# Kernel optimization log

Measured on AMD Instinct MI355X. Metric: run time of the kernel, lower is better.

Reference implementation:

```python
import jax, jax.numpy as jnp
import numpy as np

GRAPH_SIZE = 1024
D_MODEL = 256
BATCH = 32
INITIAL_ALPHA = 1.0


def setup_inputs() -> dict:
    key = jax.random.key(0)
    ks = jax.random.split(key, 10)
    s = 1.0 / np.sqrt(D_MODEL)  # torch Linear default init scale
    inp = {
        "query": jax.random.normal(ks[0], (BATCH, GRAPH_SIZE, D_MODEL), jnp.float32),
        "key_": jax.random.normal(ks[1], (BATCH, GRAPH_SIZE, D_MODEL), jnp.float32),
        "value": jax.random.normal(ks[2], (BATCH, GRAPH_SIZE, D_MODEL), jnp.float32),
        "dist": jax.random.uniform(ks[3], (BATCH, GRAPH_SIZE, GRAPH_SIZE), jnp.float32),
        "Wq": jax.random.uniform(ks[4], (D_MODEL, D_MODEL), jnp.float32, -s, s),
        "bq": jax.random.uniform(ks[5], (D_MODEL,), jnp.float32, -s, s),
        "Wk": jax.random.uniform(ks[6], (D_MODEL, D_MODEL), jnp.float32, -s, s),
        "bk": jax.random.uniform(ks[7], (D_MODEL,), jnp.float32, -s, s),
        "Wv": jax.random.uniform(ks[8], (D_MODEL, D_MODEL), jnp.float32, -s, s),
        "bv": jax.random.uniform(ks[9], (D_MODEL,), jnp.float32, -s, s),
        # alpha_raw = exp(initial_alpha - 1)
        "alpha_raw": jnp.asarray(np.exp(INITIAL_ALPHA - 1.0), jnp.float32),
    }
    return inp


def reference(query, key_, value, dist, Wq, bq, Wk, bk, Wv, bv, alpha_raw):
    # self-attention path: mask=None, cross=False, query_size == graph_size
    log2_N = jnp.log2(jnp.asarray(GRAPH_SIZE, jnp.float32))
    alpha = jax.nn.softplus(alpha_raw) + 1e-6

    q = jnp.einsum('bnd,ed->bne', query, Wq) + bq   # fc_q
    k = jnp.einsum('bnd,ed->bne', key_, Wk) + bk    # fc_k
    v = jnp.einsum('bnd,ed->bne', value, Wv) + bv   # fc_v

    exp_A = jnp.exp(-alpha * log2_N * dist)         # [b, n, n]
    exp_K = jnp.exp(k)                              # [b, n, d]

    numerator = jnp.einsum('bqk,bkd->bqd', exp_A, exp_K * v)
    denominator = jnp.einsum('bqk,bkd->bqd', exp_A, exp_K) + 1e-8
    return jax.nn.sigmoid(q) * (numerator / denominator)
```

## Files before the change

kernel.cpp:

```cpp
#include <hip/hip_runtime.h>
#include <hip/hip_bf16.h>

#define NBATCH 32
#define NG 1024
#define DM 256
#define HB 16

typedef short bf16x8 __attribute__((ext_vector_type(8)));
typedef float f32x4 __attribute__((ext_vector_type(4)));
typedef unsigned short u16x4 __attribute__((ext_vector_type(4)));
typedef unsigned short u16x8 __attribute__((ext_vector_type(8)));

static __device__ __forceinline__ unsigned short f2bf(float f) {
    __hip_bfloat16 h = __float2bfloat16(f);
    return *reinterpret_cast<unsigned short*>(&h);
}

static __device__ __forceinline__ void gload16(const void* g, void* l) {
    __builtin_amdgcn_global_load_lds(
        (const __attribute__((address_space(1))) unsigned int*)g,
        (__attribute__((address_space(3))) unsigned int*)l, 16, 0, 0);
}

__global__ __launch_bounds__(256) void wpack_kernel(
    const float* __restrict__ Wq, const float* __restrict__ Wk,
    const float* __restrict__ Wv, unsigned short* __restrict__ Wb)
{
    const int i4 = (blockIdx.x * 256 + threadIdx.x) * 4;
    const int t = i4 >> 16;
    const int off = i4 & 65535;
    const float* src = (t == 0) ? Wq : (t == 1) ? Wk : Wv;
    float4 v = *(const float4*)(src + off);
    *(u16x4*)(Wb + i4) = (u16x4){ f2bf(v.x), f2bf(v.y), f2bf(v.z), f2bf(v.w) };
}

__global__ __launch_bounds__(256) void conv_kernel(
    const float* __restrict__ src, unsigned short* __restrict__ dst)
{
    const size_t i8 = ((size_t)blockIdx.x * 256 + threadIdx.x) * 8;
    float4 a = *(const float4*)(src + i8);
    float4 b = *(const float4*)(src + i8 + 4);
    *(u16x8*)(dst + i8) = (u16x8){ f2bf(a.x), f2bf(a.y), f2bf(a.z), f2bf(a.w),
                                   f2bf(b.x), f2bf(b.y), f2bf(b.z), f2bf(b.w) };
}

__global__ __launch_bounds__(256) void projq_kernel(
    const unsigned short* __restrict__ Xq,
    const unsigned short* __restrict__ Wb,
    const float* __restrict__ bq,
    float* __restrict__ sigq)
{
    __shared__ __align__(128) unsigned short lds[2][2][128 * 64];

    const int bid = blockIdx.x;
    const int mt = bid >> 1, nt = bid & 1;
    const int tid = threadIdx.x;
    const int w = tid >> 6, lane = tid & 63;
    const int wm = w >> 1, wn = w & 1;
    const int l15 = lane & 15, lhi = lane >> 4;
    const int lr = lane >> 3, sl = lane & 7;
    const int sp = sl ^ lr;

    const char* Abase = (const char*)(Xq + (size_t)mt * 128 * 256);
    const char* Wbase = (const char*)(Wb + (size_t)nt * 128 * 256);

    f32x4 acc[4][4];
    #pragma unroll
    for (int mi = 0; mi < 4; ++mi)
        #pragma unroll
        for (int ni = 0; ni < 4; ++ni)
            acc[mi][ni] = (f32x4){0.f, 0.f, 0.f, 0.f};

    auto STAGE = [&](int buf, int t) {
        #pragma unroll
        for (int i = 0; i < 4; ++i) {
            const int r = w * 32 + i * 8 + lr;
            gload16(Abase + (size_t)r * 512 + t * 128 + sp * 16,
                    (char*)&lds[buf][0][0] + w * 4096 + i * 1024);
            gload16(Wbase + (size_t)r * 512 + t * 128 + sp * 16,
                    (char*)&lds[buf][1][0] + w * 4096 + i * 1024);
        }
    };

    STAGE(0, 0);
    __syncthreads();

    int cur = 0;
    for (int t = 0; t < 4; ++t) {
        if (t < 3) STAGE(cur ^ 1, t + 1);
        const char* Ab = (const char*)&lds[cur][0][0];
        const char* Bb = (const char*)&lds[cur][1][0];
        #pragma unroll
        for (int kk = 0; kk < 2; ++kk) {
            bf16x8 af[4], bfr[4];
            #pragma unroll
            for (int mi = 0; mi < 4; ++mi) {
                const int tr = wm * 64 + mi * 16 + l15;
                af[mi] = *(const bf16x8*)(Ab + ((tr * 128 + kk * 64 + lhi * 16) ^ ((tr & 7) << 4)));
            }
            #pragma unroll
            for (int ni = 0; ni < 4; ++ni) {
                const int tr = wn * 64 + ni * 16 + l15;
                bfr[ni] = *(const bf16x8*)(Bb + ((tr * 128 + kk * 64 + lhi * 16) ^ ((tr & 7) << 4)));
            }
            #pragma unroll
            for (int mi = 0; mi < 4; ++mi)
                #pragma unroll
                for (int ni = 0; ni < 4; ++ni)
                    acc[mi][ni] = __builtin_amdgcn_mfma_f32_16x16x32_bf16(
                        af[mi], bfr[ni], acc[mi][ni], 0, 0, 0);
        }
        __syncthreads();
        cur ^= 1;
    }

    #pragma unroll
    for (int ni = 0; ni < 4; ++ni) {
        const int c = nt * 128 + wn * 64 + ni * 16 + l15;
        const float bqs = bq[c];
        #pragma unroll
        for (int mi = 0; mi < 4; ++mi)
            #pragma unroll
            for (int r = 0; r < 4; ++r) {
                const size_t R = (size_t)mt * 128 + wm * 64 + mi * 16 + lhi * 4 + r;
                const float qv = acc[mi][ni][r] + bqs;
                sigq[R * DM + c] = 1.0f / (1.0f + __expf(-qv));
            }
    }
}

__global__ __launch_bounds__(256) void projkv_kernel(
    const unsigned short* __restrict__ Xk,
    const unsigned short* __restrict__ Xv,
    const unsigned short* __restrict__ Wkb,
    const unsigned short* __restrict__ Wvb,
    const float* __restrict__ bk, const float* __restrict__ bv,
    unsigned short* __restrict__ Pt)
{
    __shared__ __align__(128) unsigned short lds[2][2][128 * 64];

    const int bid = blockIdx.x;
    const int mt = bid >> 1, nt = bid & 1;
    const int tid = threadIdx.x;
    const int w = tid >> 6, lane = tid & 63;
    const int wm = w >> 1, wn = w & 1;
    const int l15 = lane & 15, lhi = lane >> 4;
    const int lr = lane >> 3, sl = lane & 7;
    const int sp = sl ^ lr;
    const int g16 = (sp & 3) * 16;

    f32x4 kacc[4][4], vacc[4][4];
    #pragma unroll
    for (int mi = 0; mi < 4; ++mi)
        #pragma unroll
        for (int ni = 0; ni < 4; ++ni) {
            kacc[mi][ni] = (f32x4){0.f, 0.f, 0.f, 0.f};
            vacc[mi][ni] = (f32x4){0.f, 0.f, 0.f, 0.f};
        }

    auto STAGE = [&](int buf, int t) {
        #pragma unroll
        for (int i = 0; i < 4; ++i) {
            const int r = w * 32 + i * 8 + lr;
            const char* asrc = (sp < 4 ? (const char*)Xk : (const char*)Xv)
                               + (size_t)(mt * 128 + r) * 512 + t * 64 + g16;
            gload16(asrc, (char*)&lds[buf][0][0] + w * 4096 + i * 1024);
            const char* wsrc = (sp < 4 ? (const char*)Wkb : (const char*)Wvb)
                               + (size_t)(nt * 128 + r) * 512 + t * 64 + g16;
            gload16(wsrc, (char*)&lds[buf][1][0] + w * 4096 + i * 1024);
        }
    };

    STAGE(0, 0);
    __syncthreads();

    int cur = 0;
    for (int t = 0; t < 8; ++t) {
        if (t < 7) STAGE(cur ^ 1, t + 1);
        const char* Ab = (const char*)&lds[cur][0][0];
        const char* Bb = (const char*)&lds[cur][1][0];
        bf16x8 kaf[4], vaf[4], kbf[4], vbf[4];
        #pragma unroll
        for (int mi = 0; mi < 4; ++mi) {
            const int tr = wm * 64 + mi * 16 + l15;
            const int sw = (tr & 7) << 4;
            kaf[mi] = *(const bf16x8*)(Ab + ((tr * 128 + lhi * 16) ^ sw));
            vaf[mi] = *(const bf16x8*)(Ab + ((tr * 128 + 64 + lhi * 16) ^ sw));
        }
        #pragma unroll
        for (int ni = 0; ni < 4; ++ni) {
            const int tr = wn * 64 + ni * 16 + l15;
            const int sw = (tr & 7) << 4;
            kbf[ni] = *(const bf16x8*)(Bb + ((tr * 128 + lhi * 16) ^ sw));
            vbf[ni] = *(const bf16x8*)(Bb + ((tr * 128 + 64 + lhi * 16) ^ sw));
        }
        #pragma unroll
        for (int mi = 0; mi < 4; ++mi)
            #pragma unroll
            for (int ni = 0; ni < 4; ++ni) {
                kacc[mi][ni] = __builtin_amdgcn_mfma_f32_16x16x32_bf16(
                    kaf[mi], kbf[ni], kacc[mi][ni], 0, 0, 0);
                vacc[mi][ni] = __builtin_amdgcn_mfma_f32_16x16x32_bf16(
                    vaf[mi], vbf[ni], vacc[mi][ni], 0, 0, 0);
            }
        __syncthreads();
        cur ^= 1;
    }

    const int b = (mt * 128) >> 10;
    const int kb0 = (mt * 128) & 1023;
    #pragma unroll
    for (int ni = 0; ni < 4; ++ni) {
        const int c = nt * 128 + wn * 64 + ni * 16 + l15;
        const float bks = bk[c], bvs = bv[c];
        #pragma unroll
        for (int mi = 0; mi < 4; ++mi) {
            unsigned short p1[4], p2[4];
            #pragma unroll
            for (int r = 0; r < 4; ++r) {
                const float ek = __expf(kacc[mi][ni][r] + bks);
                const float vv = vacc[mi][ni][r] + bvs;
                p1[r] = f2bf(ek * vv);
                p2[r] = f2bf(ek);
            }
            const int kidx = kb0 + wm * 64 + mi * 16 + lhi * 4;
            *(u16x4*)&Pt[((size_t)b * 512 + 2 * c    ) * NG + kidx] =
                (u16x4){p1[0], p1[1], p1[2], p1[3]};
            *(u16x4*)&Pt[((size_t)b * 512 + 2 * c + 1) * NG + kidx] =
                (u16x4){p2[0], p2[1], p2[2], p2[3]};
        }
    }
}

__global__ __launch_bounds__(256) void exp_kernel(
    const float* __restrict__ dist, unsigned short* __restrict__ ea,
    const float* __restrict__ alpha_raw)
{
    const float alpha = log1pf(__expf(alpha_raw[0])) + 1e-6f;
    const float sc = -alpha * 10.0f * 1.44269504088896f;
    const size_t i8 = ((size_t)blockIdx.x * 256 + threadIdx.x) * 8;
    float4 v0 = *(const float4*)(dist + i8);
    float4 v1 = *(const float4*)(dist + i8 + 4);
    u16x8 o = { f2bf(exp2f(sc * v0.x)), f2bf(exp2f(sc * v0.y)),
                f2bf(exp2f(sc * v0.z)), f2bf(exp2f(sc * v0.w)),
                f2bf(exp2f(sc * v1.x)), f2bf(exp2f(sc * v1.y)),
                f2bf(exp2f(sc * v1.z)), f2bf(exp2f(sc * v1.w)) };
    *(u16x8*)(ea + i8) = o;
}

__global__ __launch_bounds__(256) void attn_kernel(
    const unsigned short* __restrict__ ea,
    const unsigned short* __restrict__ Pt,
    float* __restrict__ out)
{
    __shared__ __align__(128) unsigned short lds[2][2][128 * 64];

    const int bid = blockIdx.x;
    const int l = (bid & 7) * 64 + (bid >> 3);
    const int b = l >> 5;
    const int m = (l >> 2) & 7;
    const int n = l & 3;

    const int tid = threadIdx.x;
    const int w = tid >> 6, lane = tid & 63;
    const int wm = w >> 1, wn = w & 1;
    const int l15 = lane & 15, lhi = lane >> 4;
    const int lr = lane >> 3, cb = lane & 7;
    const int cbs = cb ^ lr;

    const char* Abase = (const char*)(ea + ((size_t)b * NG + m * 128) * NG);
    const char* Bbase = (const char*)(Pt + ((size_t)b * 512 + n * 128) * NG);

    f32x4 acc[4][4];
    #pragma unroll
    for (int mi = 0; mi < 4; ++mi)
        #pragma unroll
        for (int ni = 0; ni < 4; ++ni)
            acc[mi][ni] = (f32x4){0.f, 0.f, 0.f, 0.f};

    auto STAGE = [&](int buf, int t) {
        #pragma unroll
        for (int i = 0; i < 4; ++i) {
            const int r = w * 32 + i * 8 + lr;
            const size_t goff = (size_t)r * 2048 + t * 128 + cbs * 16;
            char* ldst = (char*)&lds[buf][0][0] + w * 4096 + i * 1024;
            gload16(Abase + goff, ldst);
            gload16(Bbase + goff, ldst + 16384);
        }
    };

    STAGE(0, 0);
    __syncthreads();

    int cur = 0;
    for (int t = 0; t < 16; ++t) {
        if (t < 15) STAGE(cur ^ 1, t + 1);
        const char* Ab = (const char*)&lds[cur][0][0];
        const char* Bb = (const char*)&lds[cur][1][0];
        #pragma unroll
        for (int kk = 0; kk < 2; ++kk) {
            const int bc = kk * 64 + lhi * 16;
            bf16x8 af[4], bfr[4];
            #pragma unroll
            for (int mi = 0; mi < 4; ++mi) {
                const int tr = wm * 64 + mi * 16 + l15;
                af[mi] = *(const bf16x8*)(Ab + ((tr * 128 + bc) ^ ((tr & 7) << 4)));
            }
            #pragma unroll
            for (int ni = 0; ni < 4; ++ni) {
                const int tr = wn * 64 + ni * 16 + l15;
                bfr[ni] = *(const bf16x8*)(Bb + ((tr * 128 + bc) ^ ((tr & 7) << 4)));
            }
            #pragma unroll
            for (int mi = 0; mi < 4; ++mi)
                #pragma unroll
                for (int ni = 0; ni < 4; ++ni)
                    acc[mi][ni] = __builtin_amdgcn_mfma_f32_16x16x32_bf16(
                        af[mi], bfr[ni], acc[mi][ni], 0, 0, 0);
        }
        __syncthreads();
        cur ^= 1;
    }

    const int parity = lane & 1;
    #pragma unroll
    for (int mi = 0; mi < 4; ++mi)
        #pragma unroll
        for (int ni = 0; ni < 4; ++ni)
            #pragma unroll
            for (int r = 0; r < 4; ++r) {
                const float own = acc[mi][ni][r];
                const float other = __shfl_xor(own, 1, 64);
                if (!parity) {
                    const int colg = n * 128 + wn * 64 + ni * 16 + l15;
                    const int d = colg >> 1;
                    const int rowg = m * 128 + wm * 64 + mi * 16 + lhi * 4 + r;
                    const size_t idx = ((size_t)b * NG + rowg) * DM + d;
                    out[idx] = out[idx] * (own / (other + 1e-8f));
                }
            }
}

extern "C" void kernel_launch(void* const* d_in, const int* in_sizes, int n_in,
                              void* d_out, int out_size, void* d_ws, size_t ws_size,
                              hipStream_t stream) {
    const float* query = (const float*)d_in[0];
    const float* key_  = (const float*)d_in[1];
    const float* value = (const float*)d_in[2];
    const float* dist  = (const float*)d_in[3];
    const float* Wq = (const float*)d_in[4];
    const float* bq = (const float*)d_in[5];
    const float* Wk = (const float*)d_in[6];
    const float* bk = (const float*)d_in[7];
    const float* Wv = (const float*)d_in[8];
    const float* bv = (const float*)d_in[9];
    const float* alpha_raw = (const float*)d_in[10];
    float* out = (float*)d_out;

    unsigned short* Pt = (unsigned short*)d_ws;
    unsigned short* exp_buf =
        (unsigned short*)((char*)d_ws + (size_t)NBATCH * 512 * NG * sizeof(unsigned short));
    unsigned short* Wb = exp_buf + (size_t)HB * NG * NG;

    const size_t XN = (size_t)NBATCH * NG * DM;

    wpack_kernel<<<dim3(192), dim3(256), 0, stream>>>(Wq, Wk, Wv, Wb);

    conv_kernel<<<dim3(4096), dim3(256), 0, stream>>>(query, exp_buf);
    projq_kernel<<<dim3(512), dim3(256), 0, stream>>>(exp_buf, Wb, bq, out);

    unsigned short* Xk = exp_buf;
    unsigned short* Xv = exp_buf + XN;
    conv_kernel<<<dim3(4096), dim3(256), 0, stream>>>(key_, Xk);
    conv_kernel<<<dim3(4096), dim3(256), 0, stream>>>(value, Xv);
    projkv_kernel<<<dim3(512), dim3(256), 0, stream>>>(
        Xk, Xv, Wb + 65536, Wb + 131072, bk, bv, Pt);

    for (int h = 0; h < 2; ++h) {
        exp_kernel<<<dim3(8192), dim3(256), 0, stream>>>(
            dist + (size_t)h * HB * NG * NG, exp_buf, alpha_raw);
        attn_kernel<<<dim3(512), dim3(256), 0, stream>>>(
            exp_buf, Pt + (size_t)h * HB * 512 * NG, out + (size_t)h * HB * NG * DM);
    }
}
```

Measured before the change: 194.5 us.

## Overlap prefetch with compute via vmcnt waits and merge batch-halves into single launches

The GEMM main loops replace __syncthreads after staging with an explicit s_waitcnt vmcnt(8) plus barrier, so the next tile's global-to-LDS loads stay in flight while the current tile is computed. The three conversion kernels become one launch. The two batch halves of exp and attention become single launches over the full batch, which needs a larger workspace for the full exp buffer and separate conversion buffers. This cuts launch count and synchronisation stalls but depends on the vmcnt count matching the number of outstanding loads and on the workspace being large enough.

```diff
diff --git a/kernel.cpp b/kernel.cpp
--- a/kernel.cpp
+++ b/kernel.cpp
@@ -4,7 +4,6 @@
 #define NBATCH 32
 #define NG 1024
 #define DM 256
-#define HB 16
 
 typedef short bf16x8 __attribute__((ext_vector_type(8)));
 typedef float f32x4 __attribute__((ext_vector_type(4)));
@@ -20,6 +19,20 @@
     __builtin_amdgcn_global_load_lds(
         (const __attribute__((address_space(1))) unsigned int*)g,
         (__attribute__((address_space(3))) unsigned int*)l, 16, 0, 0);
+}
+
+static __device__ __forceinline__ void wait_vm8_bar() {
+    asm volatile("s_waitcnt vmcnt(8)" ::: "memory");
+    asm volatile("s_barrier" ::: "memory");
+    __builtin_amdgcn_sched_barrier(0);
+}
+static __device__ __forceinline__ void wait_vm0_bar() {
+    asm volatile("s_waitcnt vmcnt(0)" ::: "memory");
+    asm volatile("s_barrier" ::: "memory");
+    __builtin_amdgcn_sched_barrier(0);
+}
+static __device__ __forceinline__ void bar_only() {
+    asm volatile("s_barrier" ::: "memory");
 }
 
 __global__ __launch_bounds__(256) void wpack_kernel(
@@ -34,202 +47,18 @@
     *(u16x4*)(Wb + i4) = (u16x4){ f2bf(v.x), f2bf(v.y), f2bf(v.z), f2bf(v.w) };
 }
 
-__global__ __launch_bounds__(256) void conv_kernel(
-    const float* __restrict__ src, unsigned short* __restrict__ dst)
-{
-    const size_t i8 = ((size_t)blockIdx.x * 256 + threadIdx.x) * 8;
+__global__ __launch_bounds__(256) void conv3_kernel(
+    const float* __restrict__ q, const float* __restrict__ k,
+    const float* __restrict__ v, unsigned short* __restrict__ Xb)
+{
+    const int sel = blockIdx.x >> 12;
+    const float* src = (sel == 0) ? q : (sel == 1) ? k : v;
+    const size_t i8 = (((size_t)(blockIdx.x & 4095)) * 256 + threadIdx.x) * 8;
     float4 a = *(const float4*)(src + i8);
     float4 b = *(const float4*)(src + i8 + 4);
-    *(u16x8*)(dst + i8) = (u16x8){ f2bf(a.x), f2bf(a.y), f2bf(a.z), f2bf(a.w),
-                                   f2bf(b.x), f2bf(b.y), f2bf(b.z), f2bf(b.w) };
-}
-
-__global__ __launch_bounds__(256) void projq_kernel(
-    const unsigned short* __restrict__ Xq,
-    const unsigned short* __restrict__ Wb,
-    const float* __restrict__ bq,
-    float* __restrict__ sigq)
-{
-    __shared__ __align__(128) unsigned short lds[2][2][128 * 64];
-
-    const int bid = blockIdx.x;
-    const int mt = bid >> 1, nt = bid & 1;
-    const int tid = threadIdx.x;
-    const int w = tid >> 6, lane = tid & 63;
-    const int wm = w >> 1, wn = w & 1;
-    const int l15 = lane & 15, lhi = lane >> 4;
-    const int lr = lane >> 3, sl = lane & 7;
-    const int sp = sl ^ lr;
-
-    const char* Abase = (const char*)(Xq + (size_t)mt * 128 * 256);
-    const char* Wbase = (const char*)(Wb + (size_t)nt * 128 * 256);
-
-    f32x4 acc[4][4];
-    #pragma unroll
-    for (int mi = 0; mi < 4; ++mi)
-        #pragma unroll
-        for (int ni = 0; ni < 4; ++ni)
-            acc[mi][ni] = (f32x4){0.f, 0.f, 0.f, 0.f};
-
-    auto STAGE = [&](int buf, int t) {
-        #pragma unroll
-        for (int i = 0; i < 4; ++i) {
-            const int r = w * 32 + i * 8 + lr;
-            gload16(Abase + (size_t)r * 512 + t * 128 + sp * 16,
-                    (char*)&lds[buf][0][0] + w * 4096 + i * 1024);
-            gload16(Wbase + (size_t)r * 512 + t * 128 + sp * 16,
-                    (char*)&lds[buf][1][0] + w * 4096 + i * 1024);
-        }
-    };
-
-    STAGE(0, 0);
-    __syncthreads();
-
-    int cur = 0;
-    for (int t = 0; t < 4; ++t) {
-        if (t < 3) STAGE(cur ^ 1, t + 1);
-        const char* Ab = (const char*)&lds[cur][0][0];
-        const char* Bb = (const char*)&lds[cur][1][0];
-        #pragma unroll
-        for (int kk = 0; kk < 2; ++kk) {
-            bf16x8 af[4], bfr[4];
-            #pragma unroll
-            for (int mi = 0; mi < 4; ++mi) {
-                const int tr = wm * 64 + mi * 16 + l15;
-                af[mi] = *(const bf16x8*)(Ab + ((tr * 128 + kk * 64 + lhi * 16) ^ ((tr & 7) << 4)));
-            }
-            #pragma unroll
-            for (int ni = 0; ni < 4; ++ni) {
-                const int tr = wn * 64 + ni * 16 + l15;
-                bfr[ni] = *(const bf16x8*)(Bb + ((tr * 128 + kk * 64 + lhi * 16) ^ ((tr & 7) << 4)));
-            }
-            #pragma unroll
-            for (int mi = 0; mi < 4; ++mi)
-                #pragma unroll
-                for (int ni = 0; ni < 4; ++ni)
-                    acc[mi][ni] = __builtin_amdgcn_mfma_f32_16x16x32_bf16(
-                        af[mi], bfr[ni], acc[mi][ni], 0, 0, 0);
-        }
-        __syncthreads();
-        cur ^= 1;
-    }
-
-    #pragma unroll
-    for (int ni = 0; ni < 4; ++ni) {
-        const int c = nt * 128 + wn * 64 + ni * 16 + l15;
-        const float bqs = bq[c];
-        #pragma unroll
-        for (int mi = 0; mi < 4; ++mi)
-            #pragma unroll
-            for (int r = 0; r < 4; ++r) {
-                const size_t R = (size_t)mt * 128 + wm * 64 + mi * 16 + lhi * 4 + r;
-                const float qv = acc[mi][ni][r] + bqs;
-                sigq[R * DM + c] = 1.0f / (1.0f + __expf(-qv));
-            }
-    }
-}
-
-__global__ __launch_bounds__(256) void projkv_kernel(
-    const unsigned short* __restrict__ Xk,
-    const unsigned short* __restrict__ Xv,
-    const unsigned short* __restrict__ Wkb,
-    const unsigned short* __restrict__ Wvb,
-    const float* __restrict__ bk, const float* __restrict__ bv,
-    unsigned short* __restrict__ Pt)
-{
-    __shared__ __align__(128) unsigned short lds[2][2][128 * 64];
-
-    const int bid = blockIdx.x;
-    const int mt = bid >> 1, nt = bid & 1;
-    const int tid = threadIdx.x;
-    const int w = tid >> 6, lane = tid & 63;
-    const int wm = w >> 1, wn = w & 1;
-    const int l15 = lane & 15, lhi = lane >> 4;
-    const int lr = lane >> 3, sl = lane & 7;
-    const int sp = sl ^ lr;
-    const int g16 = (sp & 3) * 16;
-
-    f32x4 kacc[4][4], vacc[4][4];
-    #pragma unroll
-    for (int mi = 0; mi < 4; ++mi)
-        #pragma unroll
-        for (int ni = 0; ni < 4; ++ni) {
-            kacc[mi][ni] = (f32x4){0.f, 0.f, 0.f, 0.f};
-            vacc[mi][ni] = (f32x4){0.f, 0.f, 0.f, 0.f};
-        }
-
-    auto STAGE = [&](int buf, int t) {
-        #pragma unroll
-        for (int i = 0; i < 4; ++i) {
-            const int r = w * 32 + i * 8 + lr;
-            const char* asrc = (sp < 4 ? (const char*)Xk : (const char*)Xv)
-                               + (size_t)(mt * 128 + r) * 512 + t * 64 + g16;
-            gload16(asrc, (char*)&lds[buf][0][0] + w * 4096 + i * 1024);
-            const char* wsrc = (sp < 4 ? (const char*)Wkb : (const char*)Wvb)
-                               + (size_t)(nt * 128 + r) * 512 + t * 64 + g16;
-            gload16(wsrc, (char*)&lds[buf][1][0] + w * 4096 + i * 1024);
-        }
-    };
-
-    STAGE(0, 0);
-    __syncthreads();
-
-    int cur = 0;
-    for (int t = 0; t < 8; ++t) {
-        if (t < 7) STAGE(cur ^ 1, t + 1);
-        const char* Ab = (const char*)&lds[cur][0][0];
-        const char* Bb = (const char*)&lds[cur][1][0];
-        bf16x8 kaf[4], vaf[4], kbf[4], vbf[4];
-        #pragma unroll
-        for (int mi = 0; mi < 4; ++mi) {
-            const int tr = wm * 64 + mi * 16 + l15;
-            const int sw = (tr & 7) << 4;
-            kaf[mi] = *(const bf16x8*)(Ab + ((tr * 128 + lhi * 16) ^ sw));
-            vaf[mi] = *(const bf16x8*)(Ab + ((tr * 128 + 64 + lhi * 16) ^ sw));
-        }
-        #pragma unroll
-        for (int ni = 0; ni < 4; ++ni) {
-            const int tr = wn * 64 + ni * 16 + l15;
-            const int sw = (tr & 7) << 4;
-            kbf[ni] = *(const bf16x8*)(Bb + ((tr * 128 + lhi * 16) ^ sw));
-            vbf[ni] = *(const bf16x8*)(Bb + ((tr * 128 + 64 + lhi * 16) ^ sw));
-        }
-        #pragma unroll
-        for (int mi = 0; mi < 4; ++mi)
-            #pragma unroll
-            for (int ni = 0; ni < 4; ++ni) {
-                kacc[mi][ni] = __builtin_amdgcn_mfma_f32_16x16x32_bf16(
-                    kaf[mi], kbf[ni], kacc[mi][ni], 0, 0, 0);
-                vacc[mi][ni] = __builtin_amdgcn_mfma_f32_16x16x32_bf16(
-                    vaf[mi], vbf[ni], vacc[mi][ni], 0, 0, 0);
-            }
-        __syncthreads();
-        cur ^= 1;
-    }
-
-    const int b = (mt * 128) >> 10;
-    const int kb0 = (mt * 128) & 1023;
-    #pragma unroll
-    for (int ni = 0; ni < 4; ++ni) {
-        const int c = nt * 128 + wn * 64 + ni * 16 + l15;
-        const float bks = bk[c], bvs = bv[c];
-        #pragma unroll
-        for (int mi = 0; mi < 4; ++mi) {
-            unsigned short p1[4], p2[4];
-            #pragma unroll
-            for (int r = 0; r < 4; ++r) {
-                const float ek = __expf(kacc[mi][ni][r] + bks);
-                const float vv = vacc[mi][ni][r] + bvs;
-                p1[r] = f2bf(ek * vv);
-                p2[r] = f2bf(ek);
-            }
-            const int kidx = kb0 + wm * 64 + mi * 16 + lhi * 4;
-            *(u16x4*)&Pt[((size_t)b * 512 + 2 * c    ) * NG + kidx] =
-                (u16x4){p1[0], p1[1], p1[2], p1[3]};
-            *(u16x4*)&Pt[((size_t)b * 512 + 2 * c + 1) * NG + kidx] =
-                (u16x4){p2[0], p2[1], p2[2], p2[3]};
-        }
-    }
+    *(u16x8*)(Xb + (size_t)sel * NBATCH * NG * DM + i8) =
+        (u16x8){ f2bf(a.x), f2bf(a.y), f2bf(a.z), f2bf(a.w),
+                 f2bf(b.x), f2bf(b.y), f2bf(b.z), f2bf(b.w) };
 }
 
 __global__ __launch_bounds__(256) void exp_kernel(
@@ -248,6 +77,192 @@
     *(u16x8*)(ea + i8) = o;
 }
 
+__global__ __launch_bounds__(256) void projq_kernel(
+    const unsigned short* __restrict__ Xq,
+    const unsigned short* __restrict__ Wb,
+    const float* __restrict__ bq,
+    float* __restrict__ sigq)
+{
+    __shared__ __align__(128) unsigned short lds[2][2][128 * 64];
+
+    const int bid = blockIdx.x;
+    const int mt = bid >> 1, nt = bid & 1;
+    const int tid = threadIdx.x;
+    const int w = tid >> 6, lane = tid & 63;
+    const int wm = w >> 1, wn = w & 1;
+    const int l15 = lane & 15, lhi = lane >> 4;
+    const int lr = lane >> 3, sl = lane & 7;
+    const int sp = sl ^ lr;
+
+    const char* Abase = (const char*)(Xq + (size_t)mt * 128 * 256);
+    const char* Wbase = (const char*)(Wb + (size_t)nt * 128 * 256);
+
+    f32x4 acc[4][4];
+    #pragma unroll
+    for (int mi = 0; mi < 4; ++mi)
+        #pragma unroll
+        for (int ni = 0; ni < 4; ++ni)
+            acc[mi][ni] = (f32x4){0.f, 0.f, 0.f, 0.f};
+
+    auto STAGE = [&](int buf, int t) {
+        #pragma unroll
+        for (int i = 0; i < 4; ++i) {
+            const int r = w * 32 + i * 8 + lr;
+            gload16(Abase + (size_t)r * 512 + t * 128 + sp * 16,
+                    (char*)&lds[buf][0][0] + w * 4096 + i * 1024);
+            gload16(Wbase + (size_t)r * 512 + t * 128 + sp * 16,
+                    (char*)&lds[buf][1][0] + w * 4096 + i * 1024);
+        }
+    };
+
+    STAGE(0, 0);
+    int cur = 0;
+    for (int t = 0; t < 4; ++t) {
+        if (t < 3) { STAGE(cur ^ 1, t + 1); wait_vm8_bar(); }
+        else       { wait_vm0_bar(); }
+        const char* Ab = (const char*)&lds[cur][0][0];
+        const char* Bb = (const char*)&lds[cur][1][0];
+        #pragma unroll
+        for (int kk = 0; kk < 2; ++kk) {
+            bf16x8 af[4], bfr[4];
+            #pragma unroll
+            for (int mi = 0; mi < 4; ++mi) {
+                const int tr = wm * 64 + mi * 16 + l15;
+                af[mi] = *(const bf16x8*)(Ab + ((tr * 128 + kk * 64 + lhi * 16) ^ ((tr & 7) << 4)));
+            }
+            #pragma unroll
+            for (int ni = 0; ni < 4; ++ni) {
+                const int tr = wn * 64 + ni * 16 + l15;
+                bfr[ni] = *(const bf16x8*)(Bb + ((tr * 128 + kk * 64 + lhi * 16) ^ ((tr & 7) << 4)));
+            }
+            #pragma unroll
+            for (int mi = 0; mi < 4; ++mi)
+                #pragma unroll
+                for (int ni = 0; ni < 4; ++ni)
+                    acc[mi][ni] = __builtin_amdgcn_mfma_f32_16x16x32_bf16(
+                        af[mi], bfr[ni], acc[mi][ni], 0, 0, 0);
+        }
+        bar_only();
+        cur ^= 1;
+    }
+
+    #pragma unroll
+    for (int ni = 0; ni < 4; ++ni) {
+        const int c = nt * 128 + wn * 64 + ni * 16 + l15;
+        const float bqs = bq[c];
+        #pragma unroll
+        for (int mi = 0; mi < 4; ++mi)
+            #pragma unroll
+            for (int r = 0; r < 4; ++r) {
+                const size_t R = (size_t)mt * 128 + wm * 64 + mi * 16 + lhi * 4 + r;
+                const float qv = acc[mi][ni][r] + bqs;
+                sigq[R * DM + c] = 1.0f / (1.0f + __expf(-qv));
+            }
+    }
+}
+
+__global__ __launch_bounds__(256) void projkv_kernel(
+    const unsigned short* __restrict__ Xk,
+    const unsigned short* __restrict__ Xv,
+    const unsigned short* __restrict__ Wkb,
+    const unsigned short* __restrict__ Wvb,
+    const float* __restrict__ bk, const float* __restrict__ bv,
+    unsigned short* __restrict__ Pt)
+{
+    __shared__ __align__(128) unsigned short lds[2][2][128 * 64];
+
+    const int bid = blockIdx.x;
+    const int mt = bid >> 1, nt = bid & 1;
+    const int tid = threadIdx.x;
+    const int w = tid >> 6, lane = tid & 63;
+    const int wm = w >> 1, wn = w & 1;
+    const int l15 = lane & 15, lhi = lane >> 4;
+    const int lr = lane >> 3, sl = lane & 7;
+    const int sp = sl ^ lr;
+    const int g16 = (sp & 3) * 16;
+
+    f32x4 kacc[4][4], vacc[4][4];
+    #pragma unroll
+    for (int mi = 0; mi < 4; ++mi)
+        #pragma unroll
+        for (int ni = 0; ni < 4; ++ni) {
+            kacc[mi][ni] = (f32x4){0.f, 0.f, 0.f, 0.f};
+            vacc[mi][ni] = (f32x4){0.f, 0.f, 0.f, 0.f};
+        }
+
+    auto STAGE = [&](int buf, int t) {
+        #pragma unroll
+        for (int i = 0; i < 4; ++i) {
+            const int r = w * 32 + i * 8 + lr;
+            const char* asrc = (sp < 4 ? (const char*)Xk : (const char*)Xv)
+                               + (size_t)(mt * 128 + r) * 512 + t * 64 + g16;
+            gload16(asrc, (char*)&lds[buf][0][0] + w * 4096 + i * 1024);
+            const char* wsrc = (sp < 4 ? (const char*)Wkb : (const char*)Wvb)
+                               + (size_t)(nt * 128 + r) * 512 + t * 64 + g16;
+            gload16(wsrc, (char*)&lds[buf][1][0] + w * 4096 + i * 1024);
+        }
+    };
+
+    STAGE(0, 0);
+    int cur = 0;
+    for (int t = 0; t < 8; ++t) {
+        if (t < 7) { STAGE(cur ^ 1, t + 1); wait_vm8_bar(); }
+        else       { wait_vm0_bar(); }
+        const char* Ab = (const char*)&lds[cur][0][0];
+        const char* Bb = (const char*)&lds[cur][1][0];
+        bf16x8 kaf[4], vaf[4], kbf[4], vbf[4];
+        #pragma unroll
+        for (int mi = 0; mi < 4; ++mi) {
+            const int tr = wm * 64 + mi * 16 + l15;
+            const int sw = (tr & 7) << 4;
+            kaf[mi] = *(const bf16x8*)(Ab + ((tr * 128 + lhi * 16) ^ sw));
+            vaf[mi] = *(const bf16x8*)(Ab + ((tr * 128 + 64 + lhi * 16) ^ sw));
+        }
+        #pragma unroll
+        for (int ni = 0; ni < 4; ++ni) {
+            const int tr = wn * 64 + ni * 16 + l15;
+            const int sw = (tr & 7) << 4;
+            kbf[ni] = *(const bf16x8*)(Bb + ((tr * 128 + lhi * 16) ^ sw));
+            vbf[ni] = *(const bf16x8*)(Bb + ((tr * 128 + 64 + lhi * 16) ^ sw));
+        }
+        #pragma unroll
+        for (int mi = 0; mi < 4; ++mi)
+            #pragma unroll
+            for (int ni = 0; ni < 4; ++ni) {
+                kacc[mi][ni] = __builtin_amdgcn_mfma_f32_16x16x32_bf16(
+                    kaf[mi], kbf[ni], kacc[mi][ni], 0, 0, 0);
+                vacc[mi][ni] = __builtin_amdgcn_mfma_f32_16x16x32_bf16(
+                    vaf[mi], vbf[ni], vacc[mi][ni], 0, 0, 0);
+            }
+        bar_only();
+        cur ^= 1;
+    }
+
+    const int b = (mt * 128) >> 10;
+    const int kb0 = (mt * 128) & 1023;
+    #pragma unroll
+    for (int ni = 0; ni < 4; ++ni) {
+        const int c = nt * 128 + wn * 64 + ni * 16 + l15;
+        const float bks = bk[c], bvs = bv[c];
+        #pragma unroll
+        for (int mi = 0; mi < 4; ++mi) {
+            unsigned short p1[4], p2[4];
+            #pragma unroll
+            for (int r = 0; r < 4; ++r) {
+                const float ek = __expf(kacc[mi][ni][r] + bks);
+                const float vv = vacc[mi][ni][r] + bvs;
+                p1[r] = f2bf(ek * vv);
+                p2[r] = f2bf(ek);
+            }
+            const int kidx = kb0 + wm * 64 + mi * 16 + lhi * 4;
+            *(u16x4*)&Pt[((size_t)b * 512 + 2 * c    ) * NG + kidx] =
+                (u16x4){p1[0], p1[1], p1[2], p1[3]};
+            *(u16x4*)&Pt[((size_t)b * 512 + 2 * c + 1) * NG + kidx] =
+                (u16x4){p2[0], p2[1], p2[2], p2[3]};
+        }
+    }
+}
+
 __global__ __launch_bounds__(256) void attn_kernel(
     const unsigned short* __restrict__ ea,
     const unsigned short* __restrict__ Pt,
@@ -256,7 +271,7 @@
     __shared__ __align__(128) unsigned short lds[2][2][128 * 64];
 
     const int bid = blockIdx.x;
-    const int l = (bid & 7) * 64 + (bid >> 3);
+    const int l = (bid & 7) * 128 + (bid >> 3);
     const int b = l >> 5;
     const int m = (l >> 2) & 7;
     const int n = l & 3;
@@ -290,11 +305,10 @@
     };
 
     STAGE(0, 0);
-    __syncthreads();
-
     int cur = 0;
     for (int t = 0; t < 16; ++t) {
-        if (t < 15) STAGE(cur ^ 1, t + 1);
+        if (t < 15) { STAGE(cur ^ 1, t + 1); wait_vm8_bar(); }
+        else        { wait_vm0_bar(); }
         const char* Ab = (const char*)&lds[cur][0][0];
         const char* Bb = (const char*)&lds[cur][1][0];
         #pragma unroll
@@ -318,7 +332,7 @@
                     acc[mi][ni] = __builtin_amdgcn_mfma_f32_16x16x32_bf16(
                         af[mi], bfr[ni], acc[mi][ni], 0, 0, 0);
         }
-        __syncthreads();
+        bar_only();
         cur ^= 1;
     }
 
@@ -358,28 +372,18 @@
     float* out = (float*)d_out;
 
     unsigned short* Pt = (unsigned short*)d_ws;
-    unsigned short* exp_buf =
-        (unsigned short*)((char*)d_ws + (size_t)NBATCH * 512 * NG * sizeof(unsigned short));
-    unsigned short* Wb = exp_buf + (size_t)HB * NG * NG;
-
+    unsigned short* ea = Pt + (size_t)NBATCH * 512 * NG;
+    unsigned short* Xb = ea + (size_t)NBATCH * NG * NG;
     const size_t XN = (size_t)NBATCH * NG * DM;
+    unsigned short* Wb = Xb + 3 * XN;
 
     wpack_kernel<<<dim3(192), dim3(256), 0, stream>>>(Wq, Wk, Wv, Wb);
-
-    conv_kernel<<<dim3(4096), dim3(256), 0, stream>>>(query, exp_buf);
-    projq_kernel<<<dim3(512), dim3(256), 0, stream>>>(exp_buf, Wb, bq, out);
-
-    unsigned short* Xk = exp_buf;
-    unsigned short* Xv = exp_buf + XN;
-    conv_kernel<<<dim3(4096), dim3(256), 0, stream>>>(key_, Xk);
-    conv_kernel<<<dim3(4096), dim3(256), 0, stream>>>(value, Xv);
+    conv3_kernel<<<dim3(12288), dim3(256), 0, stream>>>(query, key_, value, Xb);
+
+    projq_kernel<<<dim3(512), dim3(256), 0, stream>>>(Xb, Wb, bq, out);
     projkv_kernel<<<dim3(512), dim3(256), 0, stream>>>(
-        Xk, Xv, Wb + 65536, Wb + 131072, bk, bv, Pt);
-
-    for (int h = 0; h < 2; ++h) {
-        exp_kernel<<<dim3(8192), dim3(256), 0, stream>>>(
-            dist + (size_t)h * HB * NG * NG, exp_buf, alpha_raw);
-        attn_kernel<<<dim3(512), dim3(256), 0, stream>>>(
-            exp_buf, Pt + (size_t)h * HB * 512 * NG, out + (size_t)h * HB * NG * DM);
-    }
-}
+        Xb + XN, Xb + 2 * XN, Wb + 65536, Wb + 131072, bk, bv, Pt);
+
+    exp_kernel<<<dim3(16384), dim3(256), 0, stream>>>(dist, ea, alpha_raw);
+    attn_kernel<<<dim3(1024), dim3(256), 0, stream>>>(ea, Pt, out);
+}
```

Result: no change. 195.3 us (+0.4%).
